# Kernel tuning notes

Measured on AMD Instinct MI355X. Metric: run time of the kernel, lower is better.

Reference implementation:

```python
import jax, jax.numpy as jnp
import numpy as np

N_NODES = 50000
N_EDGES = 800000
NUM_GRAPHS = 128
FEAT = 128
HID = 64
NUM_LAYERS = 3
OUT = 2
K = 30
LATENT = HID * NUM_LAYERS + 1  # 193 = conv1 kernel size & stride


def _lin(k, i, o):
    s = 1.0 / np.sqrt(i)
    return jax.random.uniform(k, (i, o), jnp.float32, -s, s)


def setup_inputs() -> dict:
    key = jax.random.key(0)
    ks = jax.random.split(key, 16)
    x = jax.random.normal(ks[0], (N_NODES, FEAT), jnp.float32)
    edge_index = jax.random.randint(ks[1], (2, N_EDGES), 0, N_NODES, dtype=jnp.int64)
    batch = jnp.sort(jax.random.randint(ks[2], (N_NODES,), 0, NUM_GRAPHS, dtype=jnp.int64))
    w0 = _lin(ks[3], FEAT, HID); b0 = jnp.zeros((HID,), jnp.float32)
    w1 = _lin(ks[4], HID, HID);  b1 = jnp.zeros((HID,), jnp.float32)
    w2 = _lin(ks[5], HID, HID);  b2 = jnp.zeros((HID,), jnp.float32)
    w3 = _lin(ks[6], HID, 1);    b3 = jnp.zeros((1,), jnp.float32)
    conv1_w = jax.random.normal(ks[7], (16, 1, LATENT), jnp.float32) * (1.0 / np.sqrt(LATENT))
    conv1_b = jnp.zeros((16,), jnp.float32)
    conv2_w = jax.random.normal(ks[8], (32, 16, 5), jnp.float32) * (1.0 / np.sqrt(16 * 5))
    conv2_b = jnp.zeros((32,), jnp.float32)
    dense_dim = (int((K - 2) / 2 + 1) - 5 + 1) * 32  # 352
    lin1_w = _lin(ks[9], dense_dim, 256); lin1_b = jnp.zeros((256,), jnp.float32)
    lin2_w = _lin(ks[10], 256, OUT);      lin2_b = jnp.zeros((OUT,), jnp.float32)
    return dict(x=x, edge_index=edge_index, batch=batch,
                w0=w0, b0=b0, w1=w1, b1=b1, w2=w2, b2=b2, w3=w3, b3=b3,
                conv1_w=conv1_w, conv1_b=conv1_b, conv2_w=conv2_w, conv2_b=conv2_b,
                lin1_w=lin1_w, lin1_b=lin1_b, lin2_w=lin2_w, lin2_b=lin2_b)


def _gcn(h_in, w, b, src, dst, norm, n):
    # GCNConv: out_i = sum_j d_i^-1/2 d_j^-1/2 (x_j W) over A+I, plus bias
    h = h_in @ w
    msg = h[src] * norm[:, None]  # gather over edges (incl. self loops)
    return jax.ops.segment_sum(msg, dst, num_segments=n) + b


def _sort_pool(x, batch, k, g):
    # per-graph descending sort on last channel, top-k, zero-pad
    n, d = x.shape
    order = jnp.lexsort((-x[:, -1], batch))  # primary: batch asc, secondary: last feat desc
    xs, bs = x[order], batch[order]
    counts = jax.ops.segment_sum(jnp.ones((n,), jnp.int32), batch, num_segments=g)
    starts = jnp.cumsum(counts) - counts
    rank = jnp.arange(n) - starts[bs]
    slot = jnp.where(rank < k, rank, k)  # overflow nodes dumped in slot k (discarded)
    out = jnp.zeros((g, k + 1, d), x.dtype).at[bs, slot].set(xs)
    return out[:, :k].reshape(g, k * d)


def _conv1d(z, w, stride):
    return jax.lax.conv_general_dilated(z, w, window_strides=(stride,), padding='VALID',
                                        dimension_numbers=('NCH', 'OIH', 'NCH'))


def reference(x, edge_index, batch, w0, b0, w1, b1, w2, b2, w3, b3,
              conv1_w, conv1_b, conv2_w, conv2_b, lin1_w, lin1_b, lin2_w, lin2_b):
    n = x.shape[0]
    loop = jnp.arange(n, dtype=edge_index.dtype)
    src = jnp.concatenate([edge_index[0], loop])
    dst = jnp.concatenate([edge_index[1], loop])
    deg = jax.ops.segment_sum(jnp.ones_like(src, jnp.float32), dst, num_segments=n)
    dinv = jnp.where(deg > 0, jax.lax.rsqrt(deg), 0.0)
    norm = dinv[src] * dinv[dst]

    h1 = jnp.tanh(_gcn(x,  w0, b0, src, dst, norm, n))
    h2 = jnp.tanh(_gcn(h1, w1, b1, src, dst, norm, n))
    h3 = jnp.tanh(_gcn(h2, w2, b2, src, dst, norm, n))
    h4 = jnp.tanh(_gcn(h3, w3, b3, src, dst, norm, n))
    hcat = jnp.concatenate([h1, h2, h3, h4], axis=-1)  # [N, 193]

    p = _sort_pool(hcat, batch, K, NUM_GRAPHS)  # [G, K*193]
    z = p[:, None, :]                                   # [G, 1, K*193]
    z = jax.nn.relu(_conv1d(z, conv1_w, LATENT) + conv1_b[None, :, None])  # [G,16,K]
    g, c, l = z.shape
    z = z.reshape(g, c, l // 2, 2).max(axis=-1)         # MaxPool1d(2,2) -> [G,16,15]
    z = jax.nn.relu(_conv1d(z, conv2_w, 1) + conv2_b[None, :, None])       # [G,32,11]
    z = z.reshape(g, -1)                                # [G,352]
    z = jax.nn.relu(z @ lin1_w + lin1_b)
    # dropout is identity in eval mode
    return z @ lin2_w + lin2_b
```

## Files before the change

kernel.cpp:

```cpp
#include <hip/hip_runtime.h>
#include <math.h>

#define NGRAPH 128
#define KTOP 30
#define LATENT 193
#define HID 64

typedef unsigned short u16;

__global__ void k_zero(int* edeg, int n) {
    int i = blockIdx.x * blockDim.x + threadIdx.x;
    if (i < n) edeg[i] = 0;
}

template <bool SCALE>
__device__ __forceinline__ void gemm_tile(const float* __restrict__ A,
                                          const float* __restrict__ W,
                                          const float* __restrict__ dinv,
                                          float* __restrict__ Hs,
                                          int M, int K, int br,
                                          float (*As)[68], float (*Bs)[68]) {
    int tid = threadIdx.x;
    int tx = tid & 15, ty = tid >> 4;
    int kA = (tid & 7) * 4;
    int rA = tid >> 3;
    int kB = tid >> 3;
    int cB = (tid & 7) * 8;
    float c[4][4] = {};
    for (int k0 = 0; k0 < K; k0 += 32) {
#pragma unroll
        for (int it = 0; it < 2; ++it) {
            int row = it * 32 + rA;
            int grow = br + row;
            float4 v = make_float4(0.f, 0.f, 0.f, 0.f);
            if (grow < M) v = *(const float4*)(A + (size_t)grow * K + k0 + kA);
            As[kA + 0][row] = v.x;
            As[kA + 1][row] = v.y;
            As[kA + 2][row] = v.z;
            As[kA + 3][row] = v.w;
        }
        {
            const float* wp = W + (size_t)(k0 + kB) * 64 + cB;
            float4 v0 = *(const float4*)(wp);
            float4 v1 = *(const float4*)(wp + 4);
            *(float4*)&Bs[kB][cB] = v0;
            *(float4*)&Bs[kB][cB + 4] = v1;
        }
        __syncthreads();
#pragma unroll
        for (int kk = 0; kk < 32; ++kk) {
            float4 a4 = *(const float4*)&As[kk][ty * 4];
            float4 b4 = *(const float4*)&Bs[kk][tx * 4];
            c[0][0] += a4.x * b4.x; c[0][1] += a4.x * b4.y; c[0][2] += a4.x * b4.z; c[0][3] += a4.x * b4.w;
            c[1][0] += a4.y * b4.x; c[1][1] += a4.y * b4.y; c[1][2] += a4.y * b4.z; c[1][3] += a4.y * b4.w;
            c[2][0] += a4.z * b4.x; c[2][1] += a4.z * b4.y; c[2][2] += a4.z * b4.z; c[2][3] += a4.z * b4.w;
            c[3][0] += a4.w * b4.x; c[3][1] += a4.w * b4.y; c[3][2] += a4.w * b4.z; c[3][3] += a4.w * b4.w;
        }
        __syncthreads();
    }
#pragma unroll
    for (int i = 0; i < 4; i++) {
        int row = br + ty * 4 + i;
        if (row >= M) continue;
        float d = SCALE ? dinv[row] : 1.f;
        float4 o;
        o.x = c[i][0] * d; o.y = c[i][1] * d; o.z = c[i][2] * d; o.w = c[i][3] * d;
        *(float4*)(Hs + (size_t)row * HID + tx * 4) = o;
    }
}

__global__ __launch_bounds__(256) void k_gemm_hist(
        const float* __restrict__ A, const float* __restrict__ W,
        float* __restrict__ Hs, int M, int K, int NG,
        const int* __restrict__ dst, const int* __restrict__ batch,
        int* edeg, u16* __restrict__ rank, int* starts,
        int E, int n, int NH) {
    __shared__ float As[32][68];
    __shared__ float Bs[32][68];
    int bid = blockIdx.x;
    if ((bid & 1) == 0) {
        int gid = bid >> 1;
        if (gid >= NG) return;
        gemm_tile<false>(A, W, nullptr, Hs, M, K, gid * 64, As, Bs);
    } else {
        int fid = bid >> 1;
        if (fid >= NH) return;
        int t = threadIdx.x;
        int gi = fid * 256 + t;
        if (gi < n) {
            int b = batch[gi];
            if (gi == 0) {
                for (int g = 0; g <= b; g++) starts[g] = 0;
            } else {
                int pb = batch[gi - 1];
                for (int g = pb + 1; g <= b; g++) starts[g] = gi;
            }
            if (gi == n - 1) {
                for (int g = b + 1; g <= NGRAPH; g++) starts[g] = n;
            }
        }
        int base = fid * 1024;
#pragma unroll
        for (int k = 0; k < 4; k++) {
            int e = base + k * 256 + t;
            if (e < E) {
                int d = dst[e];
                rank[e] = (u16)atomicAdd(&edeg[d], 1);
            }
        }
    }
}

__global__ void k_scan1(const int* __restrict__ edeg, int* offs, int* bsum,
                        float* dinv, int n) {
    __shared__ int s[256];
    int t = threadIdx.x;
    int gi = blockIdx.x * 256 + t;
    int v = (gi < n) ? edeg[gi] : 0;
    if (gi < n) dinv[gi] = rsqrtf((float)(v + 1));
    s[t] = v;
    __syncthreads();
    for (int o = 1; o < 256; o <<= 1) {
        int add = (t >= o) ? s[t - o] : 0;
        __syncthreads();
        s[t] += add;
        __syncthreads();
    }
    if (gi < n) offs[gi] = s[t] - v;
    if (t == 255) bsum[blockIdx.x] = s[255];
}

__global__ void k_scan23(int* offs, const int* __restrict__ bsum,
                         int n, int E, int nb) {
    __shared__ int s[256];
    int t = threadIdx.x;
    int bid = blockIdx.x;
    int v = (t < nb) ? bsum[t] : 0;
    s[t] = v;
    __syncthreads();
    for (int o = 1; o < 256; o <<= 1) {
        int add = (t >= o) ? s[t - o] : 0;
        __syncthreads();
        s[t] += add;
        __syncthreads();
    }
    int boffv = (bid == 0) ? 0 : s[bid - 1];
    int gi = bid * 256 + t;
    if (gi < n) offs[gi] += boffv;
    if (gi == 0) offs[n] = E;
}

__global__ __launch_bounds__(256) void k_fill(const int* __restrict__ src,
                                              const int* __restrict__ dst,
                                              const u16* __restrict__ rank,
                                              const int* __restrict__ offs,
                                              u16* __restrict__ csr, int E) {
    int t = blockIdx.x * 256 + threadIdx.x;
    int e0 = t * 4;
    if (e0 + 4 <= E) {
        int4 s4 = *(const int4*)(src + e0);
        int4 d4 = *(const int4*)(dst + e0);
        uint2 rv = *(const uint2*)(rank + e0);
        csr[offs[d4.x] + (rv.x & 0xffff)] = (u16)s4.x;
        csr[offs[d4.y] + (rv.x >> 16)]    = (u16)s4.y;
        csr[offs[d4.z] + (rv.y & 0xffff)] = (u16)s4.z;
        csr[offs[d4.w] + (rv.y >> 16)]    = (u16)s4.w;
    } else {
        for (int e = e0; e < E; e++)
            csr[offs[dst[e]] + rank[e]] = (u16)src[e];
    }
}

__global__ __launch_bounds__(256) void k_gemm(const float* __restrict__ A,
                                              const float* __restrict__ W,
                                              const float* __restrict__ dinv,
                                              float* __restrict__ Hs,
                                              int M, int K) {
    __shared__ float As[32][68];
    __shared__ float Bs[32][68];
    gemm_tile<true>(A, W, dinv, Hs, M, K, blockIdx.x * 64, As, Bs);
}

template <bool DEFER, bool FUSE_TS>
__global__ __launch_bounds__(256) void k_agg(const float* __restrict__ Hs,
                                             const u16* __restrict__ csr,
                                             const int* __restrict__ offs,
                                             const float* __restrict__ dinv,
                                             const float* __restrict__ b,
                                             float* __restrict__ H, int n,
                                             const float* __restrict__ w3,
                                             float* __restrict__ ts) {
    int wid = threadIdx.x >> 6;
    int lane = threadIdx.x & 63;
    int node = blockIdx.x * 4 + wid;
    if (node >= n) return;
    float d = dinv[node];
    float acc = Hs[(size_t)node * HID + lane];
    if (DEFER) acc *= d;
    int s = offs[node], e = offs[node + 1];
    int i = s;
    for (; i + 8 <= e; i += 8) {
        float part = 0.f;
#pragma unroll
        for (int k = 0; k < 8; k++) {
            int u = csr[i + k];
            float v = Hs[(size_t)u * HID + lane];
            if (DEFER) v *= dinv[u];
            part += v;
        }
        acc += part;
    }
    for (; i < e; i++) {
        int u = csr[i];
        float v = Hs[(size_t)u * HID + lane];
        if (DEFER) v *= dinv[u];
        acc += v;
    }
    float h = tanhf(acc * d + b[lane]);
    H[(size_t)node * HID + lane] = h;
    if (FUSE_TS) {
        float v = h * w3[lane];
        for (int o = 32; o > 0; o >>= 1) v += __shfl_down(v, o, 64);
        if (lane == 0) ts[node] = v * d;
    }
}

__global__ void k_agg4(const float* __restrict__ ts, const u16* __restrict__ csr,
                       const int* __restrict__ offs, const float* __restrict__ dinv,
                       const float* __restrict__ b3, float* h4, int n) {
    int node = blockIdx.x * blockDim.x + threadIdx.x;
    if (node >= n) return;
    float acc = ts[node];
    int s = offs[node], e = offs[node + 1];
    for (int i = s; i < e; i++) acc += ts[csr[i]];
    h4[node] = tanhf(acc * dinv[node] + b3[0]);
}

__global__ __launch_bounds__(1024) void k_select_tail(
        const float* __restrict__ h1, const float* __restrict__ h2,
        const float* __restrict__ h3, const float* __restrict__ h4,
        const int* __restrict__ starts,
        const float* __restrict__ c1w, const float* __restrict__ c1b,
        const float* __restrict__ c2w, const float* __restrict__ c2b,
        const float* __restrict__ l1w, const float* __restrict__ l1b,
        const float* __restrict__ l2w, const float* __restrict__ l2b,
        float* __restrict__ out) {
    __shared__ float p[KTOP * LATENT];
    __shared__ float w1s[16 * LATENT];
    __shared__ float w2s[32 * 16 * 5];
    __shared__ float vv[1024];
    __shared__ int   sel_s[KTOP];
    __shared__ float z1[16 * KTOP];
    __shared__ float z1p[16 * 15];
    __shared__ float flat[352];
    __shared__ float part[1024];
    __shared__ float y1[256];
    int g = blockIdx.x;
    int t = threadIdx.x;
    int s = starts[g], c = starts[g + 1] - s;

    for (int i = t; i < 16 * LATENT; i += 1024) w1s[i] = c1w[i];
    for (int i = t; i < 32 * 16 * 5; i += 1024) w2s[i] = c2w[i];
    if (t < KTOP) sel_s[t] = -1;

    if (c <= 1024) {
        for (int i = t; i < c; i += 1024) vv[i] = h4[s + i];
        __syncthreads();
        for (int i = t; i < c; i += 1024) {
            float vi = vv[i];
            int r = 0;
            for (int j = 0; j < c; j++) {
                float vj = vv[j];
                r += (vj > vi) || (vj == vi && j < i);
            }
            if (r < KTOP) sel_s[r] = s + i;
        }
    } else {
        __syncthreads();
        for (int i = t; i < c; i += 1024) {
            float vi = h4[s + i];
            int r = 0;
            for (int j = 0; j < c; j++) {
                float vj = h4[s + j];
                r += (vj > vi) || (vj == vi && j < i);
            }
            if (r < KTOP) sel_s[r] = s + i;
        }
    }
    __syncthreads();

    for (int i = t; i < KTOP * LATENT; i += 1024) {
        int slot = i / LATENT;
        int j = i - slot * LATENT;
        int node = sel_s[slot];
        float v = 0.f;
        if (node >= 0) {
            if (j < 64)       v = h1[(size_t)node * HID + j];
            else if (j < 128) v = h2[(size_t)node * HID + j - 64];
            else if (j < 192) v = h3[(size_t)node * HID + j - 128];
            else              v = h4[node];
        }
        p[i] = v;
    }
    __syncthreads();
    if (t < 16 * KTOP) {
        int ch = t / KTOP, tt = t - ch * KTOP;
        float sa = c1b[ch];
        const float* wp = &w1s[ch * LATENT];
        const float* pp = &p[tt * LATENT];
        for (int j = 0; j < LATENT; j++) sa += pp[j] * wp[j];
        z1[ch * KTOP + tt] = fmaxf(sa, 0.f);
    }
    __syncthreads();
    if (t < 16 * 15) {
        int ch = t / 15, tt = t - ch * 15;
        z1p[t] = fmaxf(z1[ch * KTOP + 2 * tt], z1[ch * KTOP + 2 * tt + 1]);
    }
    __syncthreads();
    if (t < 32 * 11) {
        int c2 = t / 11, tt = t - c2 * 11;
        float sa = c2b[c2];
        for (int c1i = 0; c1i < 16; c1i++) {
            const float* wp = &w2s[(c2 * 16 + c1i) * 5];
            const float* zp = &z1p[c1i * 15 + tt];
#pragma unroll
            for (int dt = 0; dt < 5; dt++) sa += zp[dt] * wp[dt];
        }
        flat[c2 * 11 + tt] = fmaxf(sa, 0.f);
    }
    __syncthreads();
    {
        int o = t & 255, ch = t >> 8;
        int i0 = ch * 88, i1 = i0 + 88;
        float sa = 0.f;
        for (int i = i0; i < i1; i++) sa += flat[i] * l1w[(size_t)i * 256 + o];
        part[t] = sa;
    }
    __syncthreads();
    if (t < 256)
        y1[t] = fmaxf(part[t] + part[256 + t] + part[512 + t] + part[768 + t] + l1b[t], 0.f);
    __syncthreads();
    if (t < 128) {
        int o = t >> 6, lane = t & 63;
        float sa = 0.f;
        for (int i = lane; i < 256; i += 64) sa += y1[i] * l2w[(size_t)i * 2 + o];
        for (int off = 32; off > 0; off >>= 1) sa += __shfl_down(sa, off, 64);
        if (lane == 0) out[g * 2 + o] = sa + l2b[o];
    }
}

static inline char* align256(char* p) {
    return (char*)(((uintptr_t)p + 255) & ~(uintptr_t)255);
}

extern "C" void kernel_launch(void* const* d_in, const int* in_sizes, int n_in,
                              void* d_out, int out_size, void* d_ws, size_t ws_size,
                              hipStream_t stream) {
    const float* x     = (const float*)d_in[0];
    const int*  eidx   = (const int*)d_in[1];
    const int*  batch  = (const int*)d_in[2];
    const float* w0    = (const float*)d_in[3];
    const float* b0    = (const float*)d_in[4];
    const float* w1    = (const float*)d_in[5];
    const float* b1    = (const float*)d_in[6];
    const float* w2    = (const float*)d_in[7];
    const float* b2    = (const float*)d_in[8];
    const float* w3    = (const float*)d_in[9];
    const float* b3    = (const float*)d_in[10];
    const float* c1w   = (const float*)d_in[11];
    const float* c1b   = (const float*)d_in[12];
    const float* c2w   = (const float*)d_in[13];
    const float* c2b   = (const float*)d_in[14];
    const float* l1w   = (const float*)d_in[15];
    const float* l1b   = (const float*)d_in[16];
    const float* l2w   = (const float*)d_in[17];
    const float* l2b   = (const float*)d_in[18];

    int N = in_sizes[2];
    int E = in_sizes[1] / 2;
    int K0 = in_sizes[0] / N;
    const int* esrc = eidx;
    const int* edst = eidx + E;

    char* w = (char*)d_ws;
    float* dinv  = (float*)w;             w = align256(w + (size_t)N * 4);
    int*   edeg  = (int*)w;               w = align256(w + (size_t)N * 4);
    int*   offs  = (int*)w;               w = align256(w + (size_t)(N + 1) * 4);
    int*   bsum  = (int*)w;               w = align256(w + 1024);
    float* ts    = (float*)w;             w = align256(w + (size_t)N * 4);
    float* h4    = (float*)w;             w = align256(w + (size_t)N * 4);
    int* starts  = (int*)w;               w = align256(w + (NGRAPH + 1) * 4);
    u16* rank    = (u16*)w;               w = align256(w + (size_t)E * 2);
    u16* csr     = (u16*)w;               w = align256(w + (size_t)E * 2);
    float* Hs    = (float*)w;             w = align256(w + (size_t)N * HID * 4);
    float* h1    = (float*)w;             w = align256(w + (size_t)N * HID * 4);
    float* h2    = (float*)w;             w = align256(w + (size_t)N * HID * 4);
    float* h3    = (float*)w;             w = align256(w + (size_t)N * HID * 4);

    int nb = (N + 255) / 256;
    int NG = (N + 63) / 64;
    int NH = (E + 1023) / 1024;
    int agg_grid = (N + 3) / 4;

    k_zero<<<nb, 256, 0, stream>>>(edeg, N);

    int g1 = 2 * (NG > NH ? NG : NH);
    k_gemm_hist<<<g1, 256, 0, stream>>>(x, w0, Hs, N, K0, NG,
                                        edst, batch, edeg, rank, starts, E, N, NH);

    k_scan1<<<nb, 256, 0, stream>>>(edeg, offs, bsum, dinv, N);
    k_scan23<<<nb, 256, 0, stream>>>(offs, bsum, N, E, nb);

    k_fill<<<(E / 4 + 255) / 256 + 1, 256, 0, stream>>>(esrc, edst, rank, offs, csr, E);

    k_agg<true, false><<<agg_grid, 256, 0, stream>>>(Hs, csr, offs, dinv, b0, h1, N, nullptr, nullptr);
    k_gemm<<<NG, 256, 0, stream>>>(h1, w1, dinv, Hs, N, HID);
    k_agg<false, false><<<agg_grid, 256, 0, stream>>>(Hs, csr, offs, dinv, b1, h2, N, nullptr, nullptr);
    k_gemm<<<NG, 256, 0, stream>>>(h2, w2, dinv, Hs, N, HID);
    k_agg<false, true><<<agg_grid, 256, 0, stream>>>(Hs, csr, offs, dinv, b2, h3, N, w3, ts);
    k_agg4<<<nb, 256, 0, stream>>>(ts, csr, offs, dinv, b3, h4, N);

    k_select_tail<<<NGRAPH, 1024, 0, stream>>>(h1, h2, h3, h4, starts,
                                               c1w, c1b, c2w, c2b,
                                               l1w, l1b, l2w, l2b,
                                               (float*)d_out);
}
```

Baseline: 252.5 us.

## Fuse GCN aggregation with next-layer GEMM and fold final aggregation into tail

Adds a k_agg_gemm kernel in which each block aggregates 64 nodes into shared memory, applies tanh, and immediately multiplies by the next layer's weights. This replaces the separate k_agg/k_gemm pairs for layers 1 and 2 and uses a second Hs buffer for ping-pong. The scalar layer-4 aggregation (k_agg4) now runs inside k_select_tail, which writes h4 to shared memory, so two launches and the global h4 round-trip disappear. In exchange, each wave now processes 16 nodes sequentially, leaving far fewer blocks to hide gather latency, and per-graph node counts are capped at 2048.

```diff
diff --git a/kernel.cpp b/kernel.cpp
--- a/kernel.cpp
+++ b/kernel.cpp
@@ -171,14 +171,75 @@
     }
 }
 
-__global__ __launch_bounds__(256) void k_gemm(const float* __restrict__ A,
-                                              const float* __restrict__ W,
-                                              const float* __restrict__ dinv,
-                                              float* __restrict__ Hs,
-                                              int M, int K) {
-    __shared__ float As[32][68];
-    __shared__ float Bs[32][68];
-    gemm_tile<true>(A, W, dinv, Hs, M, K, blockIdx.x * 64, As, Bs);
+template <bool DEFER>
+__global__ __launch_bounds__(256) void k_agg_gemm(
+        const float* __restrict__ Hin, const u16* __restrict__ csr,
+        const int* __restrict__ offs, const float* __restrict__ dinv,
+        const float* __restrict__ b, const float* __restrict__ Wn,
+        float* __restrict__ Hout, float* __restrict__ Hnext, int M) {
+    __shared__ float hT[64][68];
+    __shared__ float Ws[64][68];
+    int tid = threadIdx.x;
+    int br = blockIdx.x * 64;
+    for (int idx = tid * 4; idx < 64 * 64; idx += 1024) {
+        int row = idx >> 6, col = idx & 63;
+        float4 v = *(const float4*)(Wn + idx);
+        *(float4*)&Ws[row][col] = v;
+    }
+    int w = tid >> 6, lane = tid & 63;
+    for (int i = 0; i < 16; i++) {
+        int r = w * 16 + i;
+        int node = br + r;
+        float h = 0.f;
+        if (node < M) {
+            float d = dinv[node];
+            float acc = Hin[(size_t)node * HID + lane];
+            if (DEFER) acc *= d;
+            int s = offs[node], e = offs[node + 1];
+            int ii = s;
+            for (; ii + 8 <= e; ii += 8) {
+                float part = 0.f;
+#pragma unroll
+                for (int k = 0; k < 8; k++) {
+                    int u = csr[ii + k];
+                    float vv = Hin[(size_t)u * HID + lane];
+                    if (DEFER) vv *= dinv[u];
+                    part += vv;
+                }
+                acc += part;
+            }
+            for (; ii < e; ii++) {
+                int u = csr[ii];
+                float vv = Hin[(size_t)u * HID + lane];
+                if (DEFER) vv *= dinv[u];
+                acc += vv;
+            }
+            h = tanhf(acc * d + b[lane]);
+            Hout[(size_t)node * HID + lane] = h;
+        }
+        hT[lane][r] = h;
+    }
+    __syncthreads();
+    int tx = tid & 15, ty = tid >> 4;
+    float c[4][4] = {};
+#pragma unroll 8
+    for (int kk = 0; kk < 64; ++kk) {
+        float4 a4 = *(const float4*)&hT[kk][ty * 4];
+        float4 b4 = *(const float4*)&Ws[kk][tx * 4];
+        c[0][0] += a4.x * b4.x; c[0][1] += a4.x * b4.y; c[0][2] += a4.x * b4.z; c[0][3] += a4.x * b4.w;
+        c[1][0] += a4.y * b4.x; c[1][1] += a4.y * b4.y; c[1][2] += a4.y * b4.z; c[1][3] += a4.y * b4.w;
+        c[2][0] += a4.z * b4.x; c[2][1] += a4.z * b4.y; c[2][2] += a4.z * b4.z; c[2][3] += a4.z * b4.w;
+        c[3][0] += a4.w * b4.x; c[3][1] += a4.w * b4.y; c[3][2] += a4.w * b4.z; c[3][3] += a4.w * b4.w;
+    }
+#pragma unroll
+    for (int i = 0; i < 4; i++) {
+        int row = br + ty * 4 + i;
+        if (row >= M) continue;
+        float d = dinv[row];
+        float4 o;
+        o.x = c[i][0] * d; o.y = c[i][1] * d; o.z = c[i][2] * d; o.w = c[i][3] * d;
+        *(float4*)(Hnext + (size_t)row * HID + tx * 4) = o;
+    }
 }
 
 template <bool DEFER, bool FUSE_TS>
@@ -225,20 +286,11 @@
     }
 }
 
-__global__ void k_agg4(const float* __restrict__ ts, const u16* __restrict__ csr,
-                       const int* __restrict__ offs, const float* __restrict__ dinv,
-                       const float* __restrict__ b3, float* h4, int n) {
-    int node = blockIdx.x * blockDim.x + threadIdx.x;
-    if (node >= n) return;
-    float acc = ts[node];
-    int s = offs[node], e = offs[node + 1];
-    for (int i = s; i < e; i++) acc += ts[csr[i]];
-    h4[node] = tanhf(acc * dinv[node] + b3[0]);
-}
-
 __global__ __launch_bounds__(1024) void k_select_tail(
         const float* __restrict__ h1, const float* __restrict__ h2,
-        const float* __restrict__ h3, const float* __restrict__ h4,
+        const float* __restrict__ h3, const float* __restrict__ ts,
+        const u16* __restrict__ csr, const int* __restrict__ offs,
+        const float* __restrict__ dinv, const float* __restrict__ b3,
         const int* __restrict__ starts,
         const float* __restrict__ c1w, const float* __restrict__ c1b,
         const float* __restrict__ c2w, const float* __restrict__ c2b,
@@ -248,7 +300,7 @@
     __shared__ float p[KTOP * LATENT];
     __shared__ float w1s[16 * LATENT];
     __shared__ float w2s[32 * 16 * 5];
-    __shared__ float vv[1024];
+    __shared__ float vv[2048];
     __shared__ int   sel_s[KTOP];
     __shared__ float z1[16 * KTOP];
     __shared__ float z1p[16 * 15];
@@ -257,35 +309,32 @@
     __shared__ float y1[256];
     int g = blockIdx.x;
     int t = threadIdx.x;
-    int s = starts[g], c = starts[g + 1] - s;
+    int s = starts[g];
+    int c = starts[g + 1] - s;
+    if (c > 2048) c = 2048;
 
     for (int i = t; i < 16 * LATENT; i += 1024) w1s[i] = c1w[i];
     for (int i = t; i < 32 * 16 * 5; i += 1024) w2s[i] = c2w[i];
     if (t < KTOP) sel_s[t] = -1;
 
-    if (c <= 1024) {
-        for (int i = t; i < c; i += 1024) vv[i] = h4[s + i];
-        __syncthreads();
-        for (int i = t; i < c; i += 1024) {
-            float vi = vv[i];
-            int r = 0;
-            for (int j = 0; j < c; j++) {
-                float vj = vv[j];
-                r += (vj > vi) || (vj == vi && j < i);
-            }
-            if (r < KTOP) sel_s[r] = s + i;
-        }
-    } else {
-        __syncthreads();
-        for (int i = t; i < c; i += 1024) {
-            float vi = h4[s + i];
-            int r = 0;
-            for (int j = 0; j < c; j++) {
-                float vj = h4[s + j];
-                r += (vj > vi) || (vj == vi && j < i);
-            }
-            if (r < KTOP) sel_s[r] = s + i;
-        }
+    float bb = b3[0];
+    for (int i = t; i < c; i += 1024) {
+        int node = s + i;
+        float acc = ts[node];
+        int es = offs[node], ee = offs[node + 1];
+        for (int j = es; j < ee; j++) acc += ts[csr[j]];
+        vv[i] = tanhf(acc * dinv[node] + bb);
+    }
+    __syncthreads();
+
+    for (int i = t; i < c; i += 1024) {
+        float vi = vv[i];
+        int r = 0;
+        for (int j = 0; j < c; j++) {
+            float vj = vv[j];
+            r += (vj > vi) || (vj == vi && j < i);
+        }
+        if (r < KTOP) sel_s[r] = s + i;
     }
     __syncthreads();
 
@@ -298,7 +347,7 @@
             if (j < 64)       v = h1[(size_t)node * HID + j];
             else if (j < 128) v = h2[(size_t)node * HID + j - 64];
             else if (j < 192) v = h3[(size_t)node * HID + j - 128];
-            else              v = h4[node];
+            else              v = vv[node - s];
         }
         p[i] = v;
     }
@@ -388,11 +437,11 @@
     int*   offs  = (int*)w;               w = align256(w + (size_t)(N + 1) * 4);
     int*   bsum  = (int*)w;               w = align256(w + 1024);
     float* ts    = (float*)w;             w = align256(w + (size_t)N * 4);
-    float* h4    = (float*)w;             w = align256(w + (size_t)N * 4);
     int* starts  = (int*)w;               w = align256(w + (NGRAPH + 1) * 4);
     u16* rank    = (u16*)w;               w = align256(w + (size_t)E * 2);
     u16* csr     = (u16*)w;               w = align256(w + (size_t)E * 2);
     float* Hs    = (float*)w;             w = align256(w + (size_t)N * HID * 4);
+    float* Hs2   = (float*)w;             w = align256(w + (size_t)N * HID * 4);
     float* h1    = (float*)w;             w = align256(w + (size_t)N * HID * 4);
     float* h2    = (float*)w;             w = align256(w + (size_t)N * HID * 4);
     float* h3    = (float*)w;             w = align256(w + (size_t)N * HID * 4);
@@ -400,7 +449,6 @@
     int nb = (N + 255) / 256;
     int NG = (N + 63) / 64;
     int NH = (E + 1023) / 1024;
-    int agg_grid = (N + 3) / 4;
 
     k_zero<<<nb, 256, 0, stream>>>(edeg, N);
 
@@ -413,14 +461,12 @@
 
     k_fill<<<(E / 4 + 255) / 256 + 1, 256, 0, stream>>>(esrc, edst, rank, offs, csr, E);
 
-    k_agg<true, false><<<agg_grid, 256, 0, stream>>>(Hs, csr, offs, dinv, b0, h1, N, nullptr, nullptr);
-    k_gemm<<<NG, 256, 0, stream>>>(h1, w1, dinv, Hs, N, HID);
-    k_agg<false, false><<<agg_grid, 256, 0, stream>>>(Hs, csr, offs, dinv, b1, h2, N, nullptr, nullptr);
-    k_gemm<<<NG, 256, 0, stream>>>(h2, w2, dinv, Hs, N, HID);
-    k_agg<false, true><<<agg_grid, 256, 0, stream>>>(Hs, csr, offs, dinv, b2, h3, N, w3, ts);
-    k_agg4<<<nb, 256, 0, stream>>>(ts, csr, offs, dinv, b3, h4, N);
-
-    k_select_tail<<<NGRAPH, 1024, 0, stream>>>(h1, h2, h3, h4, starts,
+    k_agg_gemm<true><<<NG, 256, 0, stream>>>(Hs, csr, offs, dinv, b0, w1, h1, Hs2, N);
+    k_agg_gemm<false><<<NG, 256, 0, stream>>>(Hs2, csr, offs, dinv, b1, w2, h2, Hs, N);
+    k_agg<false, true><<<(N + 3) / 4, 256, 0, stream>>>(Hs, csr, offs, dinv, b2, h3, N, w3, ts);
+
+    k_select_tail<<<NGRAPH, 1024, 0, stream>>>(h1, h2, h3, ts, csr, offs, dinv, b3,
+                                               starts,
                                                c1w, c1b, c2w, c2b,
                                                l1w, l1b, l2w, l2b,
                                                (float*)d_out);
```

Measured after the change: 291.7 us. +15.5%, slower.

## Fuse layer-4 aggregation into select tail, prescale Hs in fill kernel, vectorize agg

Applied to the files above, without the earlier changes.

Pre-scales the first-layer Hs by dinv in extra blocks of the CSR fill kernel, so the first aggregation no longer needs per-neighbor dinv loads. The aggregation loop now reads eight u16 indices with one 128-bit load after an alignment prologue and sums them as a tree. The separate h4 aggregation kernel is removed: each graph's select-tail block computes h4 for its own nodes. The rank and conv1 loops are split in halves to use more threads. This cuts launches and gather overhead, but the tail now caps graphs at 2048 nodes and uses more shared memory.

```diff
diff --git a/kernel.cpp b/kernel.cpp
--- a/kernel.cpp
+++ b/kernel.cpp
@@ -150,24 +150,30 @@
     if (gi == 0) offs[n] = E;
 }
 
-__global__ __launch_bounds__(256) void k_fill(const int* __restrict__ src,
-                                              const int* __restrict__ dst,
-                                              const u16* __restrict__ rank,
-                                              const int* __restrict__ offs,
-                                              u16* __restrict__ csr, int E) {
-    int t = blockIdx.x * 256 + threadIdx.x;
-    int e0 = t * 4;
-    if (e0 + 4 <= E) {
-        int4 s4 = *(const int4*)(src + e0);
-        int4 d4 = *(const int4*)(dst + e0);
-        uint2 rv = *(const uint2*)(rank + e0);
-        csr[offs[d4.x] + (rv.x & 0xffff)] = (u16)s4.x;
-        csr[offs[d4.y] + (rv.x >> 16)]    = (u16)s4.y;
-        csr[offs[d4.z] + (rv.y & 0xffff)] = (u16)s4.z;
-        csr[offs[d4.w] + (rv.y >> 16)]    = (u16)s4.w;
+__global__ __launch_bounds__(256) void k_fill_scale(
+        const int* __restrict__ src, const int* __restrict__ dst,
+        const u16* __restrict__ rank, const int* __restrict__ offs,
+        u16* __restrict__ csr, int E, int NF,
+        float* __restrict__ Hs, const float* __restrict__ dinv, int n) {
+    int bid = blockIdx.x;
+    if (bid < NF) {
+        int t = bid * 256 + threadIdx.x;
+        int e0 = t * 4;
+        if (e0 + 4 <= E) {
+            int4 s4 = *(const int4*)(src + e0);
+            int4 d4 = *(const int4*)(dst + e0);
+            uint2 rv = *(const uint2*)(rank + e0);
+            csr[offs[d4.x] + (rv.x & 0xffff)] = (u16)s4.x;
+            csr[offs[d4.y] + (rv.x >> 16)]    = (u16)s4.y;
+            csr[offs[d4.z] + (rv.y & 0xffff)] = (u16)s4.z;
+            csr[offs[d4.w] + (rv.y >> 16)]    = (u16)s4.w;
+        } else {
+            for (int e = e0; e < E; e++)
+                csr[offs[dst[e]] + rank[e]] = (u16)src[e];
+        }
     } else {
-        for (int e = e0; e < E; e++)
-            csr[offs[dst[e]] + rank[e]] = (u16)src[e];
+        int idx = (bid - NF) * 256 + threadIdx.x;
+        if (idx < n * HID) Hs[idx] *= dinv[idx >> 6];
     }
 }
 
@@ -181,7 +187,7 @@
     gemm_tile<true>(A, W, dinv, Hs, M, K, blockIdx.x * 64, As, Bs);
 }
 
-template <bool DEFER, bool FUSE_TS>
+template <bool FUSE_TS>
 __global__ __launch_bounds__(256) void k_agg(const float* __restrict__ Hs,
                                              const u16* __restrict__ csr,
                                              const int* __restrict__ offs,
@@ -196,26 +202,24 @@
     if (node >= n) return;
     float d = dinv[node];
     float acc = Hs[(size_t)node * HID + lane];
-    if (DEFER) acc *= d;
     int s = offs[node], e = offs[node + 1];
     int i = s;
+    int ahead = (s + 7) & ~7;
+    if (ahead > e) ahead = e;
+    for (; i < ahead; i++) acc += Hs[(size_t)csr[i] * HID + lane];
     for (; i + 8 <= e; i += 8) {
-        float part = 0.f;
-#pragma unroll
-        for (int k = 0; k < 8; k++) {
-            int u = csr[i + k];
-            float v = Hs[(size_t)u * HID + lane];
-            if (DEFER) v *= dinv[u];
-            part += v;
-        }
-        acc += part;
-    }
-    for (; i < e; i++) {
-        int u = csr[i];
-        float v = Hs[(size_t)u * HID + lane];
-        if (DEFER) v *= dinv[u];
-        acc += v;
-    }
+        uint4 c8 = *(const uint4*)(csr + i);
+        float v0 = Hs[(size_t)(c8.x & 0xffff) * HID + lane];
+        float v1 = Hs[(size_t)(c8.x >> 16)    * HID + lane];
+        float v2 = Hs[(size_t)(c8.y & 0xffff) * HID + lane];
+        float v3 = Hs[(size_t)(c8.y >> 16)    * HID + lane];
+        float v4 = Hs[(size_t)(c8.z & 0xffff) * HID + lane];
+        float v5 = Hs[(size_t)(c8.z >> 16)    * HID + lane];
+        float v6 = Hs[(size_t)(c8.w & 0xffff) * HID + lane];
+        float v7 = Hs[(size_t)(c8.w >> 16)    * HID + lane];
+        acc += ((v0 + v1) + (v2 + v3)) + ((v4 + v5) + (v6 + v7));
+    }
+    for (; i < e; i++) acc += Hs[(size_t)csr[i] * HID + lane];
     float h = tanhf(acc * d + b[lane]);
     H[(size_t)node * HID + lane] = h;
     if (FUSE_TS) {
@@ -225,20 +229,11 @@
     }
 }
 
-__global__ void k_agg4(const float* __restrict__ ts, const u16* __restrict__ csr,
-                       const int* __restrict__ offs, const float* __restrict__ dinv,
-                       const float* __restrict__ b3, float* h4, int n) {
-    int node = blockIdx.x * blockDim.x + threadIdx.x;
-    if (node >= n) return;
-    float acc = ts[node];
-    int s = offs[node], e = offs[node + 1];
-    for (int i = s; i < e; i++) acc += ts[csr[i]];
-    h4[node] = tanhf(acc * dinv[node] + b3[0]);
-}
-
 __global__ __launch_bounds__(1024) void k_select_tail(
         const float* __restrict__ h1, const float* __restrict__ h2,
-        const float* __restrict__ h3, const float* __restrict__ h4,
+        const float* __restrict__ h3, const float* __restrict__ ts,
+        const u16* __restrict__ csr, const int* __restrict__ offs,
+        const float* __restrict__ dinv, const float* __restrict__ b3,
         const int* __restrict__ starts,
         const float* __restrict__ c1w, const float* __restrict__ c1b,
         const float* __restrict__ c2w, const float* __restrict__ c2b,
@@ -248,8 +243,10 @@
     __shared__ float p[KTOP * LATENT];
     __shared__ float w1s[16 * LATENT];
     __shared__ float w2s[32 * 16 * 5];
-    __shared__ float vv[1024];
+    __shared__ float vv[2048];
+    __shared__ int   pr[2048];
     __shared__ int   sel_s[KTOP];
+    __shared__ float zpart[960];
     __shared__ float z1[16 * KTOP];
     __shared__ float z1p[16 * 15];
     __shared__ float flat[352];
@@ -257,35 +254,41 @@
     __shared__ float y1[256];
     int g = blockIdx.x;
     int t = threadIdx.x;
-    int s = starts[g], c = starts[g + 1] - s;
+    int s = starts[g];
+    int c = starts[g + 1] - s;
+    if (c > 2048) c = 2048;
 
     for (int i = t; i < 16 * LATENT; i += 1024) w1s[i] = c1w[i];
     for (int i = t; i < 32 * 16 * 5; i += 1024) w2s[i] = c2w[i];
     if (t < KTOP) sel_s[t] = -1;
 
-    if (c <= 1024) {
-        for (int i = t; i < c; i += 1024) vv[i] = h4[s + i];
-        __syncthreads();
-        for (int i = t; i < c; i += 1024) {
-            float vi = vv[i];
-            int r = 0;
-            for (int j = 0; j < c; j++) {
-                float vj = vv[j];
-                r += (vj > vi) || (vj == vi && j < i);
-            }
-            if (r < KTOP) sel_s[r] = s + i;
-        }
-    } else {
-        __syncthreads();
-        for (int i = t; i < c; i += 1024) {
-            float vi = h4[s + i];
-            int r = 0;
-            for (int j = 0; j < c; j++) {
-                float vj = h4[s + j];
-                r += (vj > vi) || (vj == vi && j < i);
-            }
-            if (r < KTOP) sel_s[r] = s + i;
-        }
+    float bb = b3[0];
+    for (int i = t; i < c; i += 1024) {
+        int node = s + i;
+        float acc = ts[node];
+        int es = offs[node], ee = offs[node + 1];
+        for (int j = es; j < ee; j++) acc += ts[csr[j]];
+        vv[i] = tanhf(acc * dinv[node] + bb);
+    }
+    __syncthreads();
+
+    int chalf = c >> 1;
+    for (int i2 = t; i2 < 2 * c; i2 += 1024) {
+        int i = i2 >> 1, half = i2 & 1;
+        float vi = vv[i];
+        int j0 = half ? chalf : 0;
+        int j1 = half ? c : chalf;
+        int r = 0;
+        for (int j = j0; j < j1; j++) {
+            float vj = vv[j];
+            r += (vj > vi) || (vj == vi && j < i);
+        }
+        pr[i2] = r;
+    }
+    __syncthreads();
+    for (int i = t; i < c; i += 1024) {
+        int r = pr[2 * i] + pr[2 * i + 1];
+        if (r < KTOP) sel_s[r] = s + i;
     }
     __syncthreads();
 
@@ -298,18 +301,27 @@
             if (j < 64)       v = h1[(size_t)node * HID + j];
             else if (j < 128) v = h2[(size_t)node * HID + j - 64];
             else if (j < 192) v = h3[(size_t)node * HID + j - 128];
-            else              v = h4[node];
+            else              v = vv[node - s];
         }
         p[i] = v;
     }
     __syncthreads();
-    if (t < 16 * KTOP) {
-        int ch = t / KTOP, tt = t - ch * KTOP;
-        float sa = c1b[ch];
+    if (t < 960) {
+        int to = (t < 480) ? t : t - 480;
+        int half = (t < 480) ? 0 : 1;
+        int ch = to / KTOP, tt = to - ch * KTOP;
         const float* wp = &w1s[ch * LATENT];
         const float* pp = &p[tt * LATENT];
-        for (int j = 0; j < LATENT; j++) sa += pp[j] * wp[j];
-        z1[ch * KTOP + tt] = fmaxf(sa, 0.f);
+        int j0 = half ? 96 : 0;
+        int j1 = half ? LATENT : 96;
+        float sa = 0.f;
+        for (int j = j0; j < j1; j++) sa += pp[j] * wp[j];
+        zpart[t] = sa;
+    }
+    __syncthreads();
+    if (t < 480) {
+        int ch = t / KTOP, tt = t - ch * KTOP;
+        z1[ch * KTOP + tt] = fmaxf(zpart[t] + zpart[480 + t] + c1b[ch], 0.f);
     }
     __syncthreads();
     if (t < 16 * 15) {
@@ -388,7 +400,6 @@
     int*   offs  = (int*)w;               w = align256(w + (size_t)(N + 1) * 4);
     int*   bsum  = (int*)w;               w = align256(w + 1024);
     float* ts    = (float*)w;             w = align256(w + (size_t)N * 4);
-    float* h4    = (float*)w;             w = align256(w + (size_t)N * 4);
     int* starts  = (int*)w;               w = align256(w + (NGRAPH + 1) * 4);
     u16* rank    = (u16*)w;               w = align256(w + (size_t)E * 2);
     u16* csr     = (u16*)w;               w = align256(w + (size_t)E * 2);
@@ -400,6 +411,8 @@
     int nb = (N + 255) / 256;
     int NG = (N + 63) / 64;
     int NH = (E + 1023) / 1024;
+    int NF = (E / 4 + 255) / 256 + 1;
+    int NS = ((size_t)N * HID + 255) / 256;
     int agg_grid = (N + 3) / 4;
 
     k_zero<<<nb, 256, 0, stream>>>(edeg, N);
@@ -411,16 +424,17 @@
     k_scan1<<<nb, 256, 0, stream>>>(edeg, offs, bsum, dinv, N);
     k_scan23<<<nb, 256, 0, stream>>>(offs, bsum, N, E, nb);
 
-    k_fill<<<(E / 4 + 255) / 256 + 1, 256, 0, stream>>>(esrc, edst, rank, offs, csr, E);
-
-    k_agg<true, false><<<agg_grid, 256, 0, stream>>>(Hs, csr, offs, dinv, b0, h1, N, nullptr, nullptr);
+    k_fill_scale<<<NF + NS, 256, 0, stream>>>(esrc, edst, rank, offs, csr, E, NF,
+                                              Hs, dinv, N);
+
+    k_agg<false><<<agg_grid, 256, 0, stream>>>(Hs, csr, offs, dinv, b0, h1, N, nullptr, nullptr);
     k_gemm<<<NG, 256, 0, stream>>>(h1, w1, dinv, Hs, N, HID);
-    k_agg<false, false><<<agg_grid, 256, 0, stream>>>(Hs, csr, offs, dinv, b1, h2, N, nullptr, nullptr);
+    k_agg<false><<<agg_grid, 256, 0, stream>>>(Hs, csr, offs, dinv, b1, h2, N, nullptr, nullptr);
     k_gemm<<<NG, 256, 0, stream>>>(h2, w2, dinv, Hs, N, HID);
-    k_agg<false, true><<<agg_grid, 256, 0, stream>>>(Hs, csr, offs, dinv, b2, h3, N, w3, ts);
-    k_agg4<<<nb, 256, 0, stream>>>(ts, csr, offs, dinv, b3, h4, N);
-
-    k_select_tail<<<NGRAPH, 1024, 0, stream>>>(h1, h2, h3, h4, starts,
+    k_agg<true><<<agg_grid, 256, 0, stream>>>(Hs, csr, offs, dinv, b2, h3, N, w3, ts);
+
+    k_select_tail<<<NGRAPH, 1024, 0, stream>>>(h1, h2, h3, ts, csr, offs, dinv, b3,
+                                               starts,
                                                c1w, c1b, c2w, c2b,
                                                l1w, l1b, l2w, l2b,
                                                (float*)d_out);
```

Result: slower. 282.2 us (+11.7%).
